# Kernel tuning notes

Measured on AMD Instinct MI355X. Metric: run time of the kernel, lower is better.

The kernel has to match this reference:

```python
import jax, jax.numpy as jnp
import numpy as np

DIM = 512
H = 8
HD = DIM // H  # head_dim = 64


def setup_inputs() -> dict:
    key = jax.random.key(0)
    k1, k2, k3 = jax.random.split(key, 3)
    B, N = 16, 4096
    x = jax.random.normal(k1, (B, DIM, N), jnp.float32)
    # qkv_proj: Conv1d(dim, H*(1+2*HD), kernel=1) == linear over channels
    Wqkv = jax.random.normal(k2, (H * (1 + 2 * HD), DIM), jnp.float32) * 0.02
    bqkv = jnp.zeros((H * (1 + 2 * HD),), jnp.float32)
    # proj: Conv1d(dim, dim, kernel=1)
    Wp = jax.random.normal(k3, (DIM, DIM), jnp.float32) * 0.02
    bp = jnp.zeros((DIM,), jnp.float32)
    return {"x": x, "Wqkv": Wqkv, "bqkv": bqkv, "Wp": Wp, "bp": bp}


def reference(x, Wqkv, bqkv, Wp, bp):
    B, C, N = x.shape
    # 1x1 conv projection -> [B, H*(1+2*HD), N]
    qkv = jnp.einsum('oc,bcn->bon', Wqkv, x) + bqkv[None, :, None]
    qkv = qkv.reshape(B, H, 1 + 2 * HD, N)
    q = qkv[:, :, 0:1, :]          # [B,H,1,N]
    k = qkv[:, :, 1:1 + HD, :]     # [B,H,HD,N]
    v = qkv[:, :, 1 + HD:, :]      # [B,H,HD,N]
    scores = jax.nn.softmax(q, axis=-1)              # softmax over N
    ctx = jnp.sum(k * scores, axis=-1, keepdims=True)  # [B,H,HD,1]
    out = jax.nn.relu(v) * ctx                         # [B,H,HD,N]
    # permute/split/cat in torch == [B,H,HD,N] -> [B,N,H*HD] -> [B,C,N]
    out = out.transpose(0, 3, 1, 2).reshape(B, N, H * HD)
    out = out.transpose(0, 2, 1)                       # [B,C,N]
    out = jnp.einsum('oc,bcn->bon', Wp, out) + bp[None, :, None]
    return out
```

## Files before the change

kernel.cpp:

```cpp
#include <hip/hip_runtime.h>

#define NB 16
#define NC 512
#define NN 4096
#define NH 8

typedef __attribute__((ext_vector_type(8))) __bf16 bf16x8;
typedef __attribute__((ext_vector_type(4))) float f32x4;

__device__ __forceinline__ unsigned short f2bf(float f) {
    union { float f; unsigned u; } x; x.f = f;
    unsigned r = x.u + 0x7FFF + ((x.u >> 16) & 1);
    return (unsigned short)(r >> 16);
}
__device__ __forceinline__ float bits2f(unsigned u) {
    union { unsigned u; float f; } x; x.u = u; return x.f;
}

__global__ void pack_kernel(const float* __restrict__ Wqkv, const float* __restrict__ bqkv,
                            const float* __restrict__ Wp,
                            unsigned short* __restrict__ Wv_bf, unsigned short* __restrict__ Wp_bf,
                            float* __restrict__ bv) {
    int t = blockIdx.x * 256 + threadIdx.x;
    int j = t >> 9, c = t & 511;
    int h = j >> 6, d = j & 63;
    Wv_bf[t] = f2bf(Wqkv[((size_t)h * 129 + 65 + d) * 512 + c]);
    Wp_bf[t] = f2bf(Wp[t]);
    if (t < 512) bv[t] = bqkv[(t >> 6) * 129 + 65 + (t & 63)];
}

__global__ __launch_bounds__(256) void transpose_q_kernel(
        const float* __restrict__ x, const float* __restrict__ Wqkv,
        unsigned short* __restrict__ xT, float* __restrict__ q) {
    __shared__ unsigned int tile[512 * 17];
    __shared__ float Ws[8][512];
    __shared__ float qw[4][8][32];
    int b = blockIdx.y, n0 = blockIdx.x * 32;
    int t = threadIdx.x;

    for (int i = t; i < 4096; i += 256)
        Ws[i >> 9][i & 511] = Wqkv[(size_t)(i >> 9) * (129 * 512) + (i & 511)];
    __syncthreads();

    int k = t & 7;
    int r0 = t >> 3;
    float accq[8][4];
#pragma unroll
    for (int h = 0; h < 8; h++)
#pragma unroll
        for (int j = 0; j < 4; j++) accq[h][j] = 0.f;
    const float* xp = x + (size_t)b * NC * NN + n0 + 4 * k;
#pragma unroll 4
    for (int p = 0; p < 16; p++) {
        int c = r0 + 32 * p;
        float4 v = *(const float4*)(xp + (size_t)c * NN);
        unsigned lo = (unsigned)f2bf(v.x) | ((unsigned)f2bf(v.y) << 16);
        unsigned hi = (unsigned)f2bf(v.z) | ((unsigned)f2bf(v.w) << 16);
        tile[c * 17 + 2 * k]     = lo;
        tile[c * 17 + 2 * k + 1] = hi;
#pragma unroll
        for (int h = 0; h < 8; h++) {
            float w = Ws[h][c];
            accq[h][0] += w * v.x;
            accq[h][1] += w * v.y;
            accq[h][2] += w * v.z;
            accq[h][3] += w * v.w;
        }
    }
    int lane = t & 63, wv = t >> 6;
#pragma unroll
    for (int h = 0; h < 8; h++)
#pragma unroll
        for (int j = 0; j < 4; j++) {
            float a = accq[h][j];
            a += __shfl_xor(a, 8);
            a += __shfl_xor(a, 16);
            a += __shfl_xor(a, 32);
            accq[h][j] = a;
        }
    if (lane < 8) {
#pragma unroll
        for (int h = 0; h < 8; h++)
#pragma unroll
            for (int j = 0; j < 4; j++) qw[wv][h][4 * lane + j] = accq[h][j];
    }
    __syncthreads();
    {
        int h = t >> 5, n = t & 31;
        q[((size_t)b * 8 + h) * NN + n0 + n] =
            qw[0][h][n] + qw[1][h][n] + qw[2][h][n] + qw[3][h][n];
    }

    unsigned short* xb = xT + (size_t)b * NN * NC;
    for (int it = wv; it < 128; it += 4) {
        int cw = it >> 4, np = it & 15;
        int c = cw * 64 + lane;
        unsigned u = tile[c * 17 + np];
        int n = n0 + 2 * np;
        xb[(size_t)n * NC + c]       = (unsigned short)(u & 0xFFFFu);
        xb[(size_t)(n + 1) * NC + c] = (unsigned short)(u >> 16);
    }
}

__global__ void softmax_kernel(const float* __restrict__ q, float* __restrict__ sT) {
    int bh = blockIdx.x;
    int b = bh >> 3, h = bh & 7;
    int t = threadIdx.x;
    __shared__ float red[8];
    const float* qp = q + (size_t)bh * NN;
    float v[16];
    float mx = -1e30f;
#pragma unroll
    for (int i = 0; i < 16; i++) { v[i] = qp[t + i * 256]; mx = fmaxf(mx, v[i]); }
#pragma unroll
    for (int o = 32; o; o >>= 1) mx = fmaxf(mx, __shfl_xor(mx, o));
    if ((t & 63) == 0) red[t >> 6] = mx;
    __syncthreads();
    mx = fmaxf(fmaxf(red[0], red[1]), fmaxf(red[2], red[3]));
    float s = 0.f;
#pragma unroll
    for (int i = 0; i < 16; i++) { v[i] = __expf(v[i] - mx); s += v[i]; }
#pragma unroll
    for (int o = 32; o; o >>= 1) s += __shfl_xor(s, o);
    __syncthreads();
    if ((t & 63) == 0) red[4 + (t >> 6)] = s;
    __syncthreads();
    float inv = 1.f / (red[4] + red[5] + red[6] + red[7]);
#pragma unroll
    for (int i = 0; i < 16; i++) {
        int n = t + i * 256;
        sT[((size_t)b * NN + n) * 8 + h] = v[i] * inv;
    }
}

__global__ void xbar_kernel(const unsigned short* __restrict__ xT, const float* __restrict__ sT,
                            float* __restrict__ xbarP) {
    int b = blockIdx.y, sl = blockIdx.x;
    int t = threadIdx.x;
    int g = __builtin_amdgcn_readfirstlane(t >> 6);
    int lane = t & 63;
    int c8 = lane * 8;
    int nbase = sl * 256 + g * 64;
    float acc[8][8];
#pragma unroll
    for (int h = 0; h < 8; h++)
#pragma unroll
        for (int c = 0; c < 8; c++) acc[h][c] = 0.f;
    const unsigned short* xp = xT + ((size_t)b * NN + nbase) * NC + c8;
    const float* sp = sT + ((size_t)b * NN + nbase) * 8;
    for (int i = 0; i < 64; i++) {
        uint4 xv = *(const uint4*)(xp + (size_t)i * NC);
        float xf[8];
        xf[0] = bits2f(xv.x << 16); xf[1] = bits2f(xv.x & 0xFFFF0000u);
        xf[2] = bits2f(xv.y << 16); xf[3] = bits2f(xv.y & 0xFFFF0000u);
        xf[4] = bits2f(xv.z << 16); xf[5] = bits2f(xv.z & 0xFFFF0000u);
        xf[6] = bits2f(xv.w << 16); xf[7] = bits2f(xv.w & 0xFFFF0000u);
#pragma unroll
        for (int h = 0; h < 8; h++) {
            float s = sp[i * 8 + h];
#pragma unroll
            for (int c = 0; c < 8; c++) acc[h][c] += s * xf[c];
        }
    }
#pragma unroll
    for (int h = 0; h < 8; h++) {
        float* dst = xbarP + (((size_t)(sl * 4 + g) * NB + b) * 8 + h) * NC + c8;
        f32x4 lo = {acc[h][0], acc[h][1], acc[h][2], acc[h][3]};
        f32x4 hi = {acc[h][4], acc[h][5], acc[h][6], acc[h][7]};
        *(f32x4*)(dst) = lo;
        *(f32x4*)(dst + 4) = hi;
    }
}

__global__ void ctx_kernel(const float* __restrict__ xbarP, const float* __restrict__ Wqkv,
                           const float* __restrict__ bqkv, float* __restrict__ ctx) {
    int bh = blockIdx.x; int b = bh >> 3, h = bh & 7;
    int t = threadIdx.x;
    __shared__ float xb[512];
    for (int i = t; i < 512; i += 256) {
        float s = 0.f;
        for (int sl = 0; sl < 64; sl++) s += xbarP[(((size_t)sl * NB + b) * 8 + h) * NC + i];
        xb[i] = s;
    }
    __syncthreads();
    int d = t >> 2, sub = t & 3;
    const float* wk = Wqkv + ((size_t)h * 129 + 1 + d) * 512;
    float acc = 0.f;
    for (int i = sub * 4; i < 512; i += 16) {
        float4 w = *(const float4*)(wk + i);
        acc += w.x * xb[i] + w.y * xb[i + 1] + w.z * xb[i + 2] + w.w * xb[i + 3];
    }
    acc += __shfl_xor(acc, 1);
    acc += __shfl_xor(acc, 2);
    if (sub == 0) ctx[(size_t)b * NC + h * 64 + d] = acc + bqkv[h * 129 + 1 + d];
}

template <int MODE>
__global__ __launch_bounds__(512) void gemm_kernel(
    const unsigned short* __restrict__ A,
    const unsigned short* __restrict__ Bmat,
    const float* __restrict__ bias,
    const float* __restrict__ ctx,
    unsigned short* __restrict__ mT,
    float* __restrict__ outp)
{
    __shared__ alignas(16) unsigned short As[256 * 32];
    __shared__ alignas(16) unsigned short Bs[128 * 32];
    int b = blockIdx.z;
    int m0 = blockIdx.y * 256, n0 = blockIdx.x * 128;
    int t = threadIdx.x;
    int lane = t & 63;
    int wid = t >> 6;
    int wm = wid >> 1, wn = wid & 1;

    const unsigned short* Bb = Bmat + ((size_t)b * NN + n0) * NC;

    f32x4 acc[4][4];
#pragma unroll
    for (int i = 0; i < 4; i++)
#pragma unroll
        for (int j = 0; j < 4; j++) { f32x4 z = {0.f, 0.f, 0.f, 0.f}; acc[i][j] = z; }

    for (int kk = 0; kk < 512; kk += 32) {
        {
            int u = t, row = u >> 2, kg = u & 3;
            uint4 va = *(const uint4*)(A + (size_t)(m0 + row) * 512 + kk + kg * 8);
            *(uint4*)(As + (size_t)u * 8) = va;
            u = t + 512; row = u >> 2; kg = u & 3;
            uint4 vb = *(const uint4*)(A + (size_t)(m0 + row) * 512 + kk + kg * 8);
            *(uint4*)(As + (size_t)u * 8) = vb;
            u = t; row = u >> 2; kg = u & 3;
            uint4 vc = *(const uint4*)(Bb + (size_t)row * 512 + kk + kg * 8);
            *(uint4*)(Bs + (size_t)u * 8) = vc;
        }
        __syncthreads();
        bf16x8 af[4], bfr[4];
        int koff = (lane >> 4) * 8;
        int arow = wm * 64 + (lane & 15);
        int brow = wn * 64 + (lane & 15);
#pragma unroll
        for (int i = 0; i < 4; i++) af[i]  = *(const bf16x8*)(As + (size_t)(arow + i * 16) * 32 + koff);
#pragma unroll
        for (int j = 0; j < 4; j++) bfr[j] = *(const bf16x8*)(Bs + (size_t)(brow + j * 16) * 32 + koff);
#pragma unroll
        for (int i = 0; i < 4; i++)
#pragma unroll
            for (int j = 0; j < 4; j++)
                acc[i][j] = __builtin_amdgcn_mfma_f32_16x16x32_bf16(af[i], bfr[j], acc[i][j], 0, 0, 0);
        __syncthreads();
    }

    int g = lane >> 4, col = lane & 15;
#pragma unroll
    for (int i = 0; i < 4; i++) {
        int j0 = m0 + wm * 64 + i * 16 + g * 4;
        if (MODE == 0) {
            float4 bv4 = *(const float4*)(bias + j0);
            float4 cx4 = *(const float4*)(ctx + (size_t)b * NC + j0);
#pragma unroll
            for (int j = 0; j < 4; j++) {
                int n = n0 + wn * 64 + j * 16 + col;
                f32x4 a = acc[i][j];
                unsigned short h0 = f2bf(fmaxf(a[0] + bv4.x, 0.f) * cx4.x);
                unsigned short h1 = f2bf(fmaxf(a[1] + bv4.y, 0.f) * cx4.y);
                unsigned short h2 = f2bf(fmaxf(a[2] + bv4.z, 0.f) * cx4.z);
                unsigned short h3 = f2bf(fmaxf(a[3] + bv4.w, 0.f) * cx4.w);
                uint2 pk;
                pk.x = (unsigned)h0 | ((unsigned)h1 << 16);
                pk.y = (unsigned)h2 | ((unsigned)h3 << 16);
                *(uint2*)(mT + ((size_t)b * NN + n) * NC + j0) = pk;
            }
        } else {
            float4 bp4 = *(const float4*)(bias + j0);
#pragma unroll
            for (int j = 0; j < 4; j++) {
                int n = n0 + wn * 64 + j * 16 + col;
                f32x4 a = acc[i][j];
                float* op = outp + (size_t)b * NC * NN + (size_t)j0 * NN + n;
                op[0]              = a[0] + bp4.x;
                op[NN]             = a[1] + bp4.y;
                op[2 * (size_t)NN] = a[2] + bp4.z;
                op[3 * (size_t)NN] = a[3] + bp4.w;
            }
        }
    }
}

extern "C" void kernel_launch(void* const* d_in, const int* in_sizes, int n_in,
                              void* d_out, int out_size, void* d_ws, size_t ws_size,
                              hipStream_t stream) {
    const float* x    = (const float*)d_in[0];
    const float* Wqkv = (const float*)d_in[1];
    const float* bqkv = (const float*)d_in[2];
    const float* Wp   = (const float*)d_in[3];
    const float* bp   = (const float*)d_in[4];
    float* outp = (float*)d_out;

    char* ws = (char*)d_ws;
    unsigned short* mT = (unsigned short*)ws;
    float* sT    = (float*)(ws + 2097152);
    float* q     = (float*)(ws + 4194304);
    float* xbarP = (float*)(ws + 20971520);
    float* ctx   = (float*)(ws + 67108864);
    unsigned short* Wv_bf = (unsigned short*)(ws + 67108864 + 32768);
    unsigned short* Wp_bf = (unsigned short*)(ws + 67108864 + 32768 + 524288);
    float* bv    = (float*)(ws + 67108864 + 32768 + 1048576);
    unsigned short* xT = (unsigned short*)d_out;

    pack_kernel<<<dim3(1024), 256, 0, stream>>>(Wqkv, bqkv, Wp, Wv_bf, Wp_bf, bv);
    transpose_q_kernel<<<dim3(128, 16), 256, 0, stream>>>(x, Wqkv, xT, q);
    softmax_kernel<<<dim3(128), 256, 0, stream>>>(q, sT);
    xbar_kernel<<<dim3(16, 16), 256, 0, stream>>>(xT, sT, xbarP);
    ctx_kernel<<<dim3(128), 256, 0, stream>>>(xbarP, Wqkv, bqkv, ctx);
    gemm_kernel<0><<<dim3(32, 2, 16), 512, 0, stream>>>(Wv_bf, xT, bv, ctx, mT, nullptr);
    gemm_kernel<1><<<dim3(32, 2, 16), 512, 0, stream>>>(Wp_bf, mT, bp, nullptr, nullptr, outp);
}
```

Measured before the change: 215.6 us.

## Halve transpose tile width, swizzle LDS layout, write packed bf16 pairs

The transpose+q kernel now handles 16 tokens per block instead of 32, which doubles the grid. The shared tile is stored as [token-pair][channel] with an XOR swizzle, and the store phase writes two adjacent channels per thread as one 32-bit word instead of separate 16-bit stores. The aim is more parallelism and wider, more coalesced global writes of the bf16 transposed x. In exchange, each block reloads the 8x512 q weights for half as much work, and each global x read covers only 64 bytes per channel row.

```diff
diff --git a/kernel.cpp b/kernel.cpp
--- a/kernel.cpp
+++ b/kernel.cpp
@@ -32,32 +32,34 @@
 __global__ __launch_bounds__(256) void transpose_q_kernel(
         const float* __restrict__ x, const float* __restrict__ Wqkv,
         unsigned short* __restrict__ xT, float* __restrict__ q) {
-    __shared__ unsigned int tile[512 * 17];
+    __shared__ unsigned int tile[8][520];
     __shared__ float Ws[8][512];
-    __shared__ float qw[4][8][32];
-    int b = blockIdx.y, n0 = blockIdx.x * 32;
-    int t = threadIdx.x;
+    __shared__ float qw[4][8][16];
+    int b = blockIdx.y, n0 = blockIdx.x * 16;
+    int t = threadIdx.x;
+    int lane = t & 63, wv = t >> 6;
 
     for (int i = t; i < 4096; i += 256)
         Ws[i >> 9][i & 511] = Wqkv[(size_t)(i >> 9) * (129 * 512) + (i & 511)];
     __syncthreads();
 
-    int k = t & 7;
-    int r0 = t >> 3;
+    int k = t & 3;
+    int r0 = t >> 2;
     float accq[8][4];
 #pragma unroll
     for (int h = 0; h < 8; h++)
 #pragma unroll
         for (int j = 0; j < 4; j++) accq[h][j] = 0.f;
     const float* xp = x + (size_t)b * NC * NN + n0 + 4 * k;
-#pragma unroll 4
-    for (int p = 0; p < 16; p++) {
-        int c = r0 + 32 * p;
+#pragma unroll
+    for (int p = 0; p < 8; p++) {
+        int c = r0 + 64 * p;
         float4 v = *(const float4*)(xp + (size_t)c * NN);
         unsigned lo = (unsigned)f2bf(v.x) | ((unsigned)f2bf(v.y) << 16);
         unsigned hi = (unsigned)f2bf(v.z) | ((unsigned)f2bf(v.w) << 16);
-        tile[c * 17 + 2 * k]     = lo;
-        tile[c * 17 + 2 * k + 1] = hi;
+        int cs = c ^ (2 * ((c >> 5) & 3));
+        tile[2 * k][cs]     = lo;
+        tile[2 * k + 1][cs] = hi;
 #pragma unroll
         for (int h = 0; h < 8; h++) {
             float w = Ws[h][c];
@@ -67,38 +69,44 @@
             accq[h][3] += w * v.w;
         }
     }
-    int lane = t & 63, wv = t >> 6;
 #pragma unroll
     for (int h = 0; h < 8; h++)
 #pragma unroll
         for (int j = 0; j < 4; j++) {
             float a = accq[h][j];
+            a += __shfl_xor(a, 4);
             a += __shfl_xor(a, 8);
             a += __shfl_xor(a, 16);
             a += __shfl_xor(a, 32);
             accq[h][j] = a;
         }
-    if (lane < 8) {
+    if (lane < 4) {
 #pragma unroll
         for (int h = 0; h < 8; h++)
 #pragma unroll
             for (int j = 0; j < 4; j++) qw[wv][h][4 * lane + j] = accq[h][j];
     }
     __syncthreads();
-    {
-        int h = t >> 5, n = t & 31;
+    if (t < 128) {
+        int h = t >> 4, n = t & 15;
         q[((size_t)b * 8 + h) * NN + n0 + n] =
             qw[0][h][n] + qw[1][h][n] + qw[2][h][n] + qw[3][h][n];
     }
 
     unsigned short* xb = xT + (size_t)b * NN * NC;
-    for (int it = wv; it < 128; it += 4) {
-        int cw = it >> 4, np = it & 15;
-        int c = cw * 64 + lane;
-        unsigned u = tile[c * 17 + np];
+#pragma unroll
+    for (int it = 0; it < 8; it++) {
+        int np = wv * 2 + (it & 1);
+        int cw = it >> 1;
+        int c = cw * 128 + 2 * lane;
+        int m2 = 2 * ((c >> 5) & 3);
+        unsigned u0 = tile[np][c ^ m2];
+        unsigned u1 = tile[np][(c + 1) ^ m2];
+        unsigned rowA = (u0 & 0xFFFFu) | (u1 << 16);
+        unsigned rowB = (u0 >> 16) | (u1 & 0xFFFF0000u);
         int n = n0 + 2 * np;
-        xb[(size_t)n * NC + c]       = (unsigned short)(u & 0xFFFFu);
-        xb[(size_t)(n + 1) * NC + c] = (unsigned short)(u >> 16);
+        *(unsigned*)(xb + (size_t)n * NC + c)       = rowA;
+        *(unsigned*)(xb + (size_t)(n + 1) * NC + c) = rowB;
     }
 }
 
@@ -308,7 +316,7 @@
     unsigned short* xT = (unsigned short*)d_out;
 
     pack_kernel<<<dim3(1024), 256, 0, stream>>>(Wqkv, bqkv, Wp, Wv_bf, Wp_bf, bv);
-    transpose_q_kernel<<<dim3(128, 16), 256, 0, stream>>>(x, Wqkv, xT, q);
+    transpose_q_kernel<<<dim3(256, 16), 256, 0, stream>>>(x, Wqkv, xT, q);
     softmax_kernel<<<dim3(128), 256, 0, stream>>>(q, sT);
     xbar_kernel<<<dim3(16, 16), 256, 0, stream>>>(xT, sT, xbarP);
     ctx_kernel<<<dim3(128), 256, 0, stream>>>(xbarP, Wqkv, bqkv, ctx);
```

Result: slower. 233.7 us (+8.4%).
